# Kernel tuning notes

Measured on AMD Instinct MI355X. Metric: run time of the kernel, lower is better.

The kernel has to match this reference:

```python
import jax, jax.numpy as jnp
import numpy as np

N = 100000      # nodes
E = 1600000     # edges (avg degree 16)
D_IN, D_H, D_OUT = 128, 128, 64
EPS = 1e-5      # BatchNorm eps


def setup_inputs() -> dict:
    key = jax.random.key(0)
    ks = jax.random.split(key, 16)
    def w(k, i, o):
        return jax.random.normal(k, (i, o), jnp.float32) / np.float32(np.sqrt(i))
    inp = {
        "x": jax.random.normal(ks[0], (N, D_IN), jnp.float32),
        "edge_index": jax.random.randint(ks[1], (2, E), 0, N, dtype=jnp.int32),
        # layer 0 (SAGEConv: lin_l on aggregated neighbors w/ bias, lin_r on root w/o bias)
        "Wl0": w(ks[2], D_IN, D_H), "bl0": jax.random.normal(ks[3], (D_H,), jnp.float32) * 0.01,
        "Wr0": w(ks[4], D_IN, D_H),
        "g0": jnp.ones((D_H,), jnp.float32), "b0": jnp.zeros((D_H,), jnp.float32),
        "m0": jax.random.normal(ks[5], (D_H,), jnp.float32) * 0.1, "v0": jnp.ones((D_H,), jnp.float32),
        # layer 1
        "Wl1": w(ks[6], D_H, D_H), "bl1": jax.random.normal(ks[7], (D_H,), jnp.float32) * 0.01,
        "Wr1": w(ks[8], D_H, D_H),
        "g1": jnp.ones((D_H,), jnp.float32), "b1": jnp.zeros((D_H,), jnp.float32),
        "m1": jax.random.normal(ks[9], (D_H,), jnp.float32) * 0.1, "v1": jnp.ones((D_H,), jnp.float32),
        # layer 2 (output)
        "Wl2": w(ks[10], D_H, D_OUT), "bl2": jax.random.normal(ks[11], (D_OUT,), jnp.float32) * 0.01,
        "Wr2": w(ks[12], D_H, D_OUT),
    }
    return inp


def _sage_conv(x, src, dst, Wl, bl, Wr):
    # mean aggregation of neighbor (source) features at destination nodes
    deg = jax.ops.segment_sum(jnp.ones((src.shape[0],), x.dtype), dst, num_segments=N)
    agg = jax.ops.segment_sum(x[src], dst, num_segments=N)  # [N, d] irregular scatter-add
    agg = agg / jnp.maximum(deg, 1.0)[:, None]
    return agg @ Wl + bl + x @ Wr


def _bn(h, g, b, m, v):
    # BatchNorm1d in eval mode (running stats)
    return g * (h - m) * jax.lax.rsqrt(v + EPS) + b


def reference(x, edge_index,
              Wl0, bl0, Wr0, g0, b0, m0, v0,
              Wl1, bl1, Wr1, g1, b1, m1, v1,
              Wl2, bl2, Wr2):
    src, dst = edge_index[0], edge_index[1]
    h = jax.nn.relu(_bn(_sage_conv(x, src, dst, Wl0, bl0, Wr0), g0, b0, m0, v0))
    h = jax.nn.relu(_bn(_sage_conv(h, src, dst, Wl1, bl1, Wr1), g1, b1, m1, v1))
    h = _sage_conv(h, src, dst, Wl2, bl2, Wr2)
    return jax.nn.log_softmax(h, axis=-1)
```

## Files before the change

### kernel.cpp

```cpp
#include <hip/hip_runtime.h>

constexpr float EPS = 1e-5f;

#define NPB_LOG 9
#define NPB 512

typedef __attribute__((ext_vector_type(8))) __bf16 bf16x8;
typedef __attribute__((ext_vector_type(4))) float f32x4;
typedef __attribute__((ext_vector_type(2))) float f32x2;

__device__ __forceinline__ float blo(unsigned u) { return __uint_as_float(u << 16); }
__device__ __forceinline__ float bhi(unsigned u) { return __uint_as_float(u & 0xffff0000u); }
__device__ __forceinline__ unsigned bf1(float f) {
    unsigned u = __float_as_uint(f);
    return (u + 0x7fffu + ((u >> 16) & 1u)) >> 16;
}
__device__ __forceinline__ unsigned pack2(float a, float b) { return bf1(a) | (bf1(b) << 16); }

__device__ __forceinline__ f32x2 fp8lo(unsigned w) {
    return __builtin_amdgcn_cvt_pk_f32_fp8(w, false);
}
__device__ __forceinline__ f32x2 fp8hi(unsigned w) {
    return __builtin_amdgcn_cvt_pk_f32_fp8(w, true);
}


__global__ void bucket_hist_kernel(const int* __restrict__ dst, int* __restrict__ bcnt,
                                   int E, int B) {
    __shared__ int h[256];
    int t = threadIdx.x;
    h[t] = 0;
    __syncthreads();
    int E4 = E >> 2;
    const uint4* d4 = reinterpret_cast<const uint4*>(dst);
    for (int i = blockIdx.x * blockDim.x + t; i < E4; i += gridDim.x * blockDim.x) {
        uint4 d = d4[i];
        atomicAdd(&h[d.x >> NPB_LOG], 1);
        atomicAdd(&h[d.y >> NPB_LOG], 1);
        atomicAdd(&h[d.z >> NPB_LOG], 1);
        atomicAdd(&h[d.w >> NPB_LOG], 1);
    }
    if (blockIdx.x == 0 && t < (E & 3))
        atomicAdd(&h[dst[E4 * 4 + t] >> NPB_LOG], 1);
    __syncthreads();
    if (t < B && h[t]) atomicAdd(&bcnt[t], h[t]);
}

__global__ void bucket_scan_kernel(const int* __restrict__ bcnt, int* __restrict__ bstart,
                                   int* __restrict__ cursorB, int B, int E) {
    __shared__ int tmp[256];
    int t = threadIdx.x;
    int v = (t < B) ? bcnt[t] : 0;
    tmp[t] = v;
    __syncthreads();
    for (int off = 1; off < 256; off <<= 1) {
        int x = tmp[t];
        if (t >= off) x += tmp[t - off];
        __syncthreads();
        tmp[t] = x;
        __syncthreads();
    }
    if (t < B) {
        int ex = tmp[t] - v;
        bstart[t] = ex;
        cursorB[t] = ex;
    }
    if (t == 0) bstart[B] = E;
}

__global__ __launch_bounds__(256) void partition_kernel(
    const int* __restrict__ src, const int* __restrict__ dst,
    int* __restrict__ cursorB, unsigned* __restrict__ ebuf, int E, int B) {
    __shared__ int hist[256];
    __shared__ int base[256];
    int t = threadIdx.x;
    hist[t] = 0;
// ... 117 lines not shown
}

__device__ __forceinline__ void swz_one(const float* __restrict__ Wl, const float* __restrict__ Wr,
                                        unsigned short* __restrict__ out, int CL, int CR, int id) {
    int C = CL + CR;
    int CT = C >> 4;
    int lane = id & 63;
    int ctkt = id >> 6;
    int ct = ctkt % CT;
    int kt = ctkt / CT;
    int col = ct * 16 + (lane & 15);
    int k0 = kt * 32 + (lane >> 4) * 8;
#pragma unroll
    for (int i = 0; i < 8; ++i) {
        int k = k0 + i;
        float w = (col < CL) ? Wl[(size_t)k * CL + col] : Wr[(size_t)k * CR + (col - CL)];
        out[(size_t)id * 8 + i] = (unsigned short)bf1(w);
    }
}

__global__ void prep_kernel(const float* __restrict__ Wl0, const float* __restrict__ Wr0,
                            const float* __restrict__ Wl1, const float* __restrict__ Wr1,
                            const float* __restrict__ Wl2, const float* __restrict__ Wr2,
                            const float* __restrict__ g0, const float* __restrict__ b0,
                            const float* __restrict__ m0, const float* __restrict__ v0,
                            const float* __restrict__ g1, const float* __restrict__ b1,
                            const float* __restrict__ m1, const float* __restrict__ v1,
                            unsigned short* __restrict__ Wsw0, unsigned short* __restrict__ Wsw1,
                            unsigned short* __restrict__ Wsw2,
                            float* __restrict__ bnA0, float* __restrict__ bnB0,
                            float* __restrict__ bnA1, float* __restrict__ bnB1) {
    int bid = blockIdx.x;
    int t = threadIdx.x;
    if (bid < 16) {
        swz_one(Wl0, Wr0, Wsw0, 128, 128, bid * 256 + t);
    } else if (bid < 32) {
        swz_one(Wl1, Wr1, Wsw1, 128, 128, (bid - 16) * 256 + t);
    } else if (bid < 40) {
        swz_one(Wl2, Wr2, Wsw2, 64, 64, (bid - 32) * 256 + t);
    } else {
        if (t < 128) {
            float A = g0[t] * rsqrtf(v0[t] + EPS);
            bnA0[t] = A;
            bnB0[t] = b0[t] - m0[t] * A;
        } else {
            int c = t - 128;
            float A = g1[c] * rsqrtf(v1[c] + EPS);
            bnA1[c] = A;
            bnB1[c] = b1[c] - m1[c] * A;
        }
    }
}

template <int CHALF, bool AF32>
__global__ __launch_bounds__(256, 4) void gemmT_kernel(
    const void* __restrict__ Av, const unsigned short* __restrict__ Wsw,
    const float* __restrict__ bl,
    unsigned char* __restrict__ tL, unsigned short* __restrict__ tR, int n) {
    constexpr int CT = CHALF / 16;
    __shared__ unsigned short As[64][136];

    int tid = threadIdx.x;
    int lane = tid & 63;
    int wave = tid >> 6;
    int wr = wave >> 1, wc = wave & 1;
    int blk0 = blockIdx.x * 64;
    int rlo = lane & 15, kq = lane >> 4;

    {
        int srow = tid >> 2;
        int schunk = tid & 3;
        int grow = blk0 + srow;
        uint4 w0 = make_uint4(0, 0, 0, 0), w1 = w0, w2 = w0, w3 = w0;
        if (grow < n) {
            if (AF32) {
                const float* Af = (const float*)Av;
                const float4* p = reinterpret_cast<const float4*>(Af + (size_t)grow * 128 + schunk * 32);
                float4 f0 = p[0], f1 = p[1], f2 = p[2], f3 = p[3];
                float4 f4 = p[4], f5 = p[5], f6 = p[6], f7 = p[7];
                w0 = make_uint4(pack2(f0.x, f0.y), pack2(f0.z, f0.w), pack2(f1.x, f1.y), pack2(f1.z, f1.w));
                w1 = make_uint4(pack2(f2.x, f2.y), pack2(f2.z, f2.w), pack2(f3.x, f3.y), pack2(f3.z, f3.w));
                w2 = make_uint4(pack2(f4.x, f4.y), pack2(f4.z, f4.w), pack2(f5.x, f5.y), pack2(f5.z, f5.w));
                w3 = make_uint4(pack2(f6.x, f6.y), pack2(f6.z, f6.w), pack2(f7.x, f7.y), pack2(f7.z, f7.w));
            } else {
                const unsigned short* A = (const unsigned short*)Av;
                const uint4* p = reinterpret_cast<const uint4*>(A + (size_t)grow * 128 + schunk * 32);
                w0 = p[0]; w1 = p[1]; w2 = p[2]; w3 = p[3];
            }
        }
        uint4* d = reinterpret_cast<uint4*>(&As[srow][schunk * 32]);
        d[0] = w0; d[1] = w1; d[2] = w2; d[3] = w3;
    }
    __syncthreads();

    f32x4 acc[2][CT];
#pragma unroll
    for (int nt = 0; nt < 2; ++nt)
#pragma unroll
        for (int c = 0; c < CT; ++c)
#pragma unroll
            for (int k = 0; k < 4; ++k) acc[nt][c][k] = 0.f;

    int lr0 = wr * 32 + rlo;
    int lr1 = wr * 32 + 16 + rlo;

    for (int kt = 0; kt < 4; ++kt) {
        int kb = kt * 32 + kq * 8;
        bf16x8 a0 = *reinterpret_cast<const bf16x8*>(&As[lr0][kb]);
        bf16x8 a1 = *reinterpret_cast<const bf16x8*>(&As[lr1][kb]);
#pragma unroll
        for (int c = 0; c < CT; ++c) {
            int ct_g = wc * CT + c;
            bf16x8 w = *reinterpret_cast<const bf16x8*>(Wsw + ((size_t)(kt * 2 * CT + ct_g) * 64 + lane) * 8);
            acc[0][c] = __builtin_amdgcn_mfma_f32_16x16x32_bf16(w, a0, acc[0][c], 0, 0, 0);
            acc[1][c] = __builtin_amdgcn_mfma_f32_16x16x32_bf16(w, a1, acc[1][c], 0, 0, 0);
        }
    }

#pragma unroll
    for (int nt = 0; nt < 2; ++nt) {
        int r = blk0 + wr * 32 + nt * 16 + rlo;
        if (r >= n) continue;
#pragma unroll
        for (int c = 0; c < CT; ++c) {
            int colbase = c * 16 + kq * 4;
            if (wc == 0) {
                unsigned w = __builtin_amdgcn_cvt_pk_fp8_f32(acc[nt][c][0], acc[nt][c][1], 0, false);
                w = __builtin_amdgcn_cvt_pk_fp8_f32(acc[nt][c][2], acc[nt][c][3], w, true);
                *reinterpret_cast<unsigned*>(tL + (size_t)r * CHALF + colbase) = w;
            } else {
                float4 bv = *reinterpret_cast<const float4*>(bl + colbase);
                uint2 o;
                o.x = pack2(acc[nt][c][0] + bv.x, acc[nt][c][1] + bv.y);
                o.y = pack2(acc[nt][c][2] + bv.z, acc[nt][c][3] + bv.w);
                *reinterpret_cast<uint2*>(tR + (size_t)r * CHALF + colbase) = o;
            }
        }
    }
}

__global__ void aggbn_kernel(const unsigned char* __restrict__ tL,
                             const unsigned short* __restrict__ tR,
                             const float* __restrict__ bnA, const float* __restrict__ bnB,
                             const int* __restrict__ rowptr, const int* __restrict__ csr,
                             const float* __restrict__ degInv,
                             unsigned short* __restrict__ h, int n) {
    int idx = blockIdx.x * blockDim.x + threadIdx.x;
    int v = idx >> 4;
    int t = idx & 15;
    if (v >= n) return;
    int beg = rowptr[v], end = rowptr[v + 1];
    const uint2* T2 = reinterpret_cast<const uint2*>(tL);
    float s0 = 0.f, s1 = 0.f, s2 = 0.f, s3 = 0.f, s4 = 0.f, s5 = 0.f, s6 = 0.f, s7 = 0.f;
    int e = beg;
    for (; e + 8 <= end; e += 8) {
        uint2 w0 = T2[(size_t)csr[e + 0] * 16 + t];
        uint2 w1 = T2[(size_t)csr[e + 1] * 16 + t];
        uint2 w2 = T2[(size_t)csr[e + 2] * 16 + t];
        uint2 w3 = T2[(size_t)csr[e + 3] * 16 + t];
        uint2 w4 = T2[(size_t)csr[e + 4] * 16 + t];
        uint2 w5 = T2[(size_t)csr[e + 5] * 16 + t];
        uint2 w6 = T2[(size_t)csr[e + 6] * 16 + t];
        uint2 w7 = T2[(size_t)csr[e + 7] * 16 + t];
        f32x2 p;
        p = fp8lo(w0.x); s0 += p[0]; s1 += p[1];
        p = fp8hi(w0.x); s2 += p[0]; s3 += p[1];
        p = fp8lo(w0.y); s4 += p[0]; s5 += p[1];
        p = fp8hi(w0.y); s6 += p[0]; s7 += p[1];
        p = fp8lo(w1.x); s0 += p[0]; s1 += p[1];
        p = fp8hi(w1.x); s2 += p[0]; s3 += p[1];
        p = fp8lo(w1.y); s4 += p[0]; s5 += p[1];
        p = fp8hi(w1.y); s6 += p[0]; s7 += p[1];
        p = fp8lo(w2.x); s0 += p[0]; s1 += p[1];
        p = fp8hi(w2.x); s2 += p[0]; s3 += p[1];
        p = fp8lo(w2.y); s4 += p[0]; s5 += p[1];
        p = fp8hi(w2.y); s6 += p[0]; s7 += p[1];
        p = fp8lo(w3.x); s0 += p[0]; s1 += p[1];
        p = fp8hi(w3.x); s2 += p[0]; s3 += p[1];
        p = fp8lo(w3.y); s4 += p[0]; s5 += p[1];
        p = fp8hi(w3.y); s6 += p[0]; s7 += p[1];
        p = fp8lo(w4.x); s0 += p[0]; s1 += p[1];
        p = fp8hi(w4.x); s2 += p[0]; s3 += p[1];
        p = fp8lo(w4.y); s4 += p[0]; s5 += p[1];
        p = fp8hi(w4.y); s6 += p[0]; s7 += p[1];
        p = fp8lo(w5.x); s0 += p[0]; s1 += p[1];
        p = fp8hi(w5.x); s2 += p[0]; s3 += p[1];
        p = fp8lo(w5.y); s4 += p[0]; s5 += p[1];
        p = fp8hi(w5.y); s6 += p[0]; s7 += p[1];
        p = fp8lo(w6.x); s0 += p[0]; s1 += p[1];
        p = fp8hi(w6.x); s2 += p[0]; s3 += p[1];
        p = fp8lo(w6.y); s4 += p[0]; s5 += p[1];
        p = fp8hi(w6.y); s6 += p[0]; s7 += p[1];
        p = fp8lo(w7.x); s0 += p[0]; s1 += p[1];
        p = fp8hi(w7.x); s2 += p[0]; s3 += p[1];
        p = fp8lo(w7.y); s4 += p[0]; s5 += p[1];
        p = fp8hi(w7.y); s6 += p[0]; s7 += p[1];
    }
    for (; e < end; ++e) {
        uint2 w = T2[(size_t)csr[e] * 16 + t];
        f32x2 p;
        p = fp8lo(w.x); s0 += p[0]; s1 += p[1];
        p = fp8hi(w.x); s2 += p[0]; s3 += p[1];
        p = fp8lo(w.y); s4 += p[0]; s5 += p[1];
        p = fp8hi(w.y); s6 += p[0]; s7 += p[1];
    }
    float di = degInv[v];
    uint4 rw = reinterpret_cast<const uint4*>(tR)[(size_t)v * 16 + t];
    float4 A0 = reinterpret_cast<const float4*>(bnA + t * 8)[0];
    float4 A1 = reinterpret_cast<const float4*>(bnA + t * 8)[1];
    float4 B0 = reinterpret_cast<const float4*>(bnB + t * 8)[0];
    float4 B1 = reinterpret_cast<const float4*>(bnB + t * 8)[1];
    float h0 = fmaxf(A0.x * (s0 * di + blo(rw.x)) + B0.x, 0.f);
    float h1 = fmaxf(A0.y * (s1 * di + bhi(rw.x)) + B0.y, 0.f);
    float h2 = fmaxf(A0.z * (s2 * di + blo(rw.y)) + B0.z, 0.f);
    float h3 = fmaxf(A0.w * (s3 * di + bhi(rw.y)) + B0.w, 0.f);
    float h4 = fmaxf(A1.x * (s4 * di + blo(rw.z)) + B1.x, 0.f);
    float h5 = fmaxf(A1.y * (s5 * di + bhi(rw.z)) + B1.y, 0.f);
    float h6 = fmaxf(A1.z * (s6 * di + blo(rw.w)) + B1.z, 0.f);
    float h7 = fmaxf(A1.w * (s7 * di + bhi(rw.w)) + B1.w, 0.f);
    uint4 o;
    o.x = pack2(h0, h1);
    o.y = pack2(h2, h3);
    o.z = pack2(h4, h5);
    o.w = pack2(h6, h7);
    reinterpret_cast<uint4*>(h)[(size_t)v * 16 + t] = o;
}

__global__ void agg64_lsm_kernel(const unsigned char* __restrict__ tL2,
                                 const unsigned short* __restrict__ tR2,
                                 const int* __restrict__ rowptr, const int* __restrict__ csr,
                                 const float* __restrict__ degInv,
                                 float* __restrict__ out, int n) {
    int idx = blockIdx.x * blockDim.x + threadIdx.x;
    int v = idx >> 3;
    int t = idx & 7;
    if (v >= n) return;
    int beg = rowptr[v], end = rowptr[v + 1];
    const uint2* T2 = reinterpret_cast<const uint2*>(tL2);
    float s0 = 0.f, s1 = 0.f, s2 = 0.f, s3 = 0.f, s4 = 0.f, s5 = 0.f, s6 = 0.f, s7 = 0.f;
    int e = beg;
    for (; e + 8 <= end; e += 8) {
        uint2 w0 = T2[(size_t)csr[e + 0] * 8 + t];
        uint2 w1 = T2[(size_t)csr[e + 1] * 8 + t];
        uint2 w2 = T2[(size_t)csr[e + 2] * 8 + t];
        uint2 w3 = T2[(size_t)csr[e + 3] * 8 + t];
        uint2 w4 = T2[(size_t)csr[e + 4] * 8 + t];
        uint2 w5 = T2[(size_t)csr[e + 5] * 8 + t];
        uint2 w6 = T2[(size_t)csr[e + 6] * 8 + t];
        uint2 w7 = T2[(size_t)csr[e + 7] * 8 + t];
        f32x2 p;
        p = fp8lo(w0.x); s0 += p[0]; s1 += p[1];
        p = fp8hi(w0.x); s2 += p[0]; s3 += p[1];
        p = fp8lo(w0.y); s4 += p[0]; s5 += p[1];
        p = fp8hi(w0.y); s6 += p[0]; s7 += p[1];
        p = fp8lo(w1.x); s0 += p[0]; s1 += p[1];
        p = fp8hi(w1.x); s2 += p[0]; s3 += p[1];
        p = fp8lo(w1.y); s4 += p[0]; s5 += p[1];
        p = fp8hi(w1.y); s6 += p[0]; s7 += p[1];
        p = fp8lo(w2.x); s0 += p[0]; s1 += p[1];
        p = fp8hi(w2.x); s2 += p[0]; s3 += p[1];
        p = fp8lo(w2.y); s4 += p[0]; s5 += p[1];
        p = fp8hi(w2.y); s6 += p[0]; s7 += p[1];
        p = fp8lo(w3.x); s0 += p[0]; s1 += p[1];
        p = fp8hi(w3.x); s2 += p[0]; s3 += p[1];
        p = fp8lo(w3.y); s4 += p[0]; s5 += p[1];
        p = fp8hi(w3.y); s6 += p[0]; s7 += p[1];
        p = fp8lo(w4.x); s0 += p[0]; s1 += p[1];
        p = fp8hi(w4.x); s2 += p[0]; s3 += p[1];
        p = fp8lo(w4.y); s4 += p[0]; s5 += p[1];
        p = fp8hi(w4.y); s6 += p[0]; s7 += p[1];
        p = fp8lo(w5.x); s0 += p[0]; s1 += p[1];
        p = fp8hi(w5.x); s2 += p[0]; s3 += p[1];
        p = fp8lo(w5.y); s4 += p[0]; s5 += p[1];
        p = fp8hi(w5.y); s6 += p[0]; s7 += p[1];
        p = fp8lo(w6.x); s0 += p[0]; s1 += p[1];
        p = fp8hi(w6.x); s2 += p[0]; s3 += p[1];
        p = fp8lo(w6.y); s4 += p[0]; s5 += p[1];
        p = fp8hi(w6.y); s6 += p[0]; s7 += p[1];
// ... 34 lines not shown
    float4 oA, oB;
    oA.x = y0 - lse; oA.y = y1 - lse; oA.z = y2 - lse; oA.w = y3 - lse;
    oB.x = y4 - lse; oB.y = y5 - lse; oB.z = y6 - lse; oB.w = y7 - lse;
    float4* O4 = reinterpret_cast<float4*>(out + (size_t)v * 64 + t * 8);
    O4[0] = oA;
    O4[1] = oB;
}


extern "C" void kernel_launch(void* const* d_in, const int* in_sizes, int n_in,
                              void* d_out, int out_size, void* d_ws, size_t ws_size,
                              hipStream_t stream) {
    const float* x   = (const float*)d_in[0];
    const int*   ei  = (const int*)d_in[1];
    const float* Wl0 = (const float*)d_in[2];
    const float* bl0 = (const float*)d_in[3];
    const float* Wr0 = (const float*)d_in[4];
    const float* g0  = (const float*)d_in[5];
    const float* b0  = (const float*)d_in[6];
    const float* m0  = (const float*)d_in[7];
    const float* v0  = (const float*)d_in[8];
    const float* Wl1 = (const float*)d_in[9];
    const float* bl1 = (const float*)d_in[10];
    const float* Wr1 = (const float*)d_in[11];
    const float* g1  = (const float*)d_in[12];
    const float* b1  = (const float*)d_in[13];
    const float* m1  = (const float*)d_in[14];
    const float* v1  = (const float*)d_in[15];
    const float* Wl2 = (const float*)d_in[16];
    const float* bl2 = (const float*)d_in[17];
    const float* Wr2 = (const float*)d_in[18];
    float* out = (float*)d_out;

    const int N = in_sizes[0] / 128;
    const int E = in_sizes[1] / 2;
    const int B = (N + NPB - 1) >> NPB_LOG;
    const int* src = ei;
    const int* dst = ei + E;

    char* ws = (char*)d_ws;
    size_t off = 0;
    auto alloc = [&](size_t bytes) -> void* {
        void* p = ws + off;
        off += (bytes + 255) & ~(size_t)255;
        return p;
    };
    int*   bcnt    = (int*)alloc(256 * 4);
    int*   bstart  = (int*)alloc(257 * 4);
    int*   cursorB = (int*)alloc(256 * 4);
    int*   rowptr  = (int*)alloc((size_t)(N + 1) * 4);
    float* degInv  = (float*)alloc((size_t)N * 4);
    int*   csr     = (int*)alloc((size_t)E * 4);
    unsigned* ebuf = (unsigned*)alloc((size_t)E * 4);
    unsigned short* hA  = (unsigned short*)alloc((size_t)N * 128 * 2);
    unsigned short* hB  = (unsigned short*)alloc((size_t)N * 128 * 2);
    unsigned char*  tL  = (unsigned char*)alloc((size_t)N * 128);
    unsigned short* tR  = (unsigned short*)alloc((size_t)N * 128 * 2);
    unsigned short* Wsw0 = (unsigned short*)alloc(4 * 16 * 64 * 8 * 2);
    unsigned short* Wsw1 = (unsigned short*)alloc(4 * 16 * 64 * 8 * 2);
    unsigned short* Wsw2 = (unsigned short*)alloc(4 * 8 * 64 * 8 * 2);
    float* bnA0 = (float*)alloc(128 * 4);
    float* bnB0 = (float*)alloc(128 * 4);
    float* bnA1 = (float*)alloc(128 * 4);
    float* bnB1 = (float*)alloc(128 * 4);
    unsigned char*  tL2 = tL;
    unsigned short* tR2 = tR;

    hipMemsetAsync(bcnt, 0, 256 * 4, stream);

    bucket_hist_kernel<<<512, 256, 0, stream>>>(dst, bcnt, E, B);
    bucket_scan_kernel<<<1, 256, 0, stream>>>(bcnt, bstart, cursorB, B, E);
    partition_kernel<<<(E + 4095) / 4096, 256, 0, stream>>>(src, dst, cursorB, ebuf, E, B);
    build_csr_kernel<<<B, 256, 0, stream>>>(ebuf, bstart, rowptr, degInv, csr, N, B);
    prep_kernel<<<41, 256, 0, stream>>>(Wl0, Wr0, Wl1, Wr1, Wl2, Wr2,
                                        g0, b0, m0, v0, g1, b1, m1, v1,
                                        Wsw0, Wsw1, Wsw2, bnA0, bnB0, bnA1, bnB1);

    int gemmGrid = (N + 63) / 64;
    int aggGrid = (int)(((size_t)N * 16 + 255) / 256);
    int lsmGrid = (int)(((size_t)N * 8 + 255) / 256);

    gemmT_kernel<128, true><<<gemmGrid, 256, 0, stream>>>(x, Wsw0, bl0, tL, tR, N);
    aggbn_kernel<<<aggGrid, 256, 0, stream>>>(tL, tR, bnA0, bnB0, rowptr, csr, degInv, hA, N);
    gemmT_kernel<128, false><<<gemmGrid, 256, 0, stream>>>(hA, Wsw1, bl1, tL, tR, N);
    aggbn_kernel<<<aggGrid, 256, 0, stream>>>(tL, tR, bnA1, bnB1, rowptr, csr, degInv, hB, N);
    gemmT_kernel<64, false><<<gemmGrid, 256, 0, stream>>>(hB, Wsw2, bl2, tL2, tR2, N);
    agg64_lsm_kernel<<<lsmGrid, 256, 0, stream>>>(tL2, tR2, rowptr, csr, degInv, out, N);
}
```

Baseline: 247.0 us.

## Fuse neighbor aggregation and BatchNorm into the following layer's GEMM kernel

```diff
diff --git a/kernel.cpp b/kernel.cpp
--- a/kernel.cpp
+++ b/kernel.cpp
@@ -22,6 +22,19 @@
 }
 __device__ __forceinline__ f32x2 fp8hi(unsigned w) {
     return __builtin_amdgcn_cvt_pk_f32_fp8(w, true);
+}
+
+template <int B>
+__device__ __forceinline__ void acc16(float (&s)[32], uint4 w) {
+    f32x2 p;
+    p = fp8lo(w.x); s[B + 0] += p[0];  s[B + 1] += p[1];
+    p = fp8hi(w.x); s[B + 2] += p[0];  s[B + 3] += p[1];
+    p = fp8lo(w.y); s[B + 4] += p[0];  s[B + 5] += p[1];
+    p = fp8hi(w.y); s[B + 6] += p[0];  s[B + 7] += p[1];
+    p = fp8lo(w.z); s[B + 8] += p[0];  s[B + 9] += p[1];
+    p = fp8hi(w.z); s[B + 10] += p[0]; s[B + 11] += p[1];
+    p = fp8lo(w.w); s[B + 12] += p[0]; s[B + 13] += p[1];
+    p = fp8hi(w.w); s[B + 14] += p[0]; s[B + 15] += p[1];
 }
 
 
@@ -245,12 +258,11 @@
     }
 }
 
-template <int CHALF, bool AF32>
-__global__ __launch_bounds__(256, 4) void gemmT_kernel(
-    const void* __restrict__ Av, const unsigned short* __restrict__ Wsw,
+__global__ __launch_bounds__(256, 4) void gemm0_kernel(
+    const float* __restrict__ Af, const unsigned short* __restrict__ Wsw,
     const float* __restrict__ bl,
     unsigned char* __restrict__ tL, unsigned short* __restrict__ tR, int n) {
-    constexpr int CT = CHALF / 16;
+    constexpr int CT = 8;
     __shared__ unsigned short As[64][136];
 
     int tid = threadIdx.x;
@@ -266,20 +278,13 @@
         int grow = blk0 + srow;
         uint4 w0 = make_uint4(0, 0, 0, 0), w1 = w0, w2 = w0, w3 = w0;
         if (grow < n) {
-            if (AF32) {
-                const float* Af = (const float*)Av;
-                const float4* p = reinterpret_cast<const float4*>(Af + (size_t)grow * 128 + schunk * 32);
-                float4 f0 = p[0], f1 = p[1], f2 = p[2], f3 = p[3];
-                float4 f4 = p[4], f5 = p[5], f6 = p[6], f7 = p[7];
-                w0 = make_uint4(pack2(f0.x, f0.y), pack2(f0.z, f0.w), pack2(f1.x, f1.y), pack2(f1.z, f1.w));
-                w1 = make_uint4(pack2(f2.x, f2.y), pack2(f2.z, f2.w), pack2(f3.x, f3.y), pack2(f3.z, f3.w));
-                w2 = make_uint4(pack2(f4.x, f4.y), pack2(f4.z, f4.w), pack2(f5.x, f5.y), pack2(f5.z, f5.w));
-                w3 = make_uint4(pack2(f6.x, f6.y), pack2(f6.z, f6.w), pack2(f7.x, f7.y), pack2(f7.z, f7.w));
-            } else {
-                const unsigned short* A = (const unsigned short*)Av;
-                const uint4* p = reinterpret_cast<const uint4*>(A + (size_t)grow * 128 + schunk * 32);
-                w0 = p[0]; w1 = p[1]; w2 = p[2]; w3 = p[3];
-            }
+            const float4* p = reinterpret_cast<const float4*>(Af + (size_t)grow * 128 + schunk * 32);
+            float4 f0 = p[0], f1 = p[1], f2 = p[2], f3 = p[3];
+            float4 f4 = p[4], f5 = p[5], f6 = p[6], f7 = p[7];
+            w0 = make_uint4(pack2(f0.x, f0.y), pack2(f0.z, f0.w), pack2(f1.x, f1.y), pack2(f1.z, f1.w));
+            w1 = make_uint4(pack2(f2.x, f2.y), pack2(f2.z, f2.w), pack2(f3.x, f3.y), pack2(f3.z, f3.w));
+            w2 = make_uint4(pack2(f4.x, f4.y), pack2(f4.z, f4.w), pack2(f5.x, f5.y), pack2(f5.z, f5.w));
+            w3 = make_uint4(pack2(f6.x, f6.y), pack2(f6.z, f6.w), pack2(f7.x, f7.y), pack2(f7.z, f7.w));
         }
         uint4* d = reinterpret_cast<uint4*>(&As[srow][schunk * 32]);
         d[0] = w0; d[1] = w1; d[2] = w2; d[3] = w3;
@@ -320,103 +325,144 @@
             if (wc == 0) {
                 unsigned w = __builtin_amdgcn_cvt_pk_fp8_f32(acc[nt][c][0], acc[nt][c][1], 0, false);
                 w = __builtin_amdgcn_cvt_pk_fp8_f32(acc[nt][c][2], acc[nt][c][3], w, true);
-                *reinterpret_cast<unsigned*>(tL + (size_t)r * CHALF + colbase) = w;
+                *reinterpret_cast<unsigned*>(tL + (size_t)r * 128 + colbase) = w;
             } else {
                 float4 bv = *reinterpret_cast<const float4*>(bl + colbase);
                 uint2 o;
                 o.x = pack2(acc[nt][c][0] + bv.x, acc[nt][c][1] + bv.y);
                 o.y = pack2(acc[nt][c][2] + bv.z, acc[nt][c][3] + bv.w);
-                *reinterpret_cast<uint2*>(tR + (size_t)r * CHALF + colbase) = o;
+                *reinterpret_cast<uint2*>(tR + (size_t)r * 128 + colbase) = o;
             }
         }
     }
 }
 
-__global__ void aggbn_kernel(const unsigned char* __restrict__ tL,
-                             const unsigned short* __restrict__ tR,
-                             const float* __restrict__ bnA, const float* __restrict__ bnB,
-                             const int* __restrict__ rowptr, const int* __restrict__ csr,
-                             const float* __restrict__ degInv,
-                             unsigned short* __restrict__ h, int n) {
-    int idx = blockIdx.x * blockDim.x + threadIdx.x;
-    int v = idx >> 4;
-    int t = idx & 15;
-    if (v >= n) return;
-    int beg = rowptr[v], end = rowptr[v + 1];
-    const uint2* T2 = reinterpret_cast<const uint2*>(tL);
-    float s0 = 0.f, s1 = 0.f, s2 = 0.f, s3 = 0.f, s4 = 0.f, s5 = 0.f, s6 = 0.f, s7 = 0.f;
-    int e = beg;
-    for (; e + 8 <= end; e += 8) {
-        uint2 w0 = T2[(size_t)csr[e + 0] * 16 + t];
-        uint2 w1 = T2[(size_t)csr[e + 1] * 16 + t];
-        uint2 w2 = T2[(size_t)csr[e + 2] * 16 + t];
-        uint2 w3 = T2[(size_t)csr[e + 3] * 16 + t];
-        uint2 w4 = T2[(size_t)csr[e + 4] * 16 + t];
-        uint2 w5 = T2[(size_t)csr[e + 5] * 16 + t];
-        uint2 w6 = T2[(size_t)csr[e + 6] * 16 + t];
-        uint2 w7 = T2[(size_t)csr[e + 7] * 16 + t];
-        f32x2 p;
-        p = fp8lo(w0.x); s0 += p[0]; s1 += p[1];
-        p = fp8hi(w0.x); s2 += p[0]; s3 += p[1];
-        p = fp8lo(w0.y); s4 += p[0]; s5 += p[1];
-        p = fp8hi(w0.y); s6 += p[0]; s7 += p[1];
-        p = fp8lo(w1.x); s0 += p[0]; s1 += p[1];
-        p = fp8hi(w1.x); s2 += p[0]; s3 += p[1];
-        p = fp8lo(w1.y); s4 += p[0]; s5 += p[1];
-        p = fp8hi(w1.y); s6 += p[0]; s7 += p[1];
-        p = fp8lo(w2.x); s0 += p[0]; s1 += p[1];
-        p = fp8hi(w2.x); s2 += p[0]; s3 += p[1];
-        p = fp8lo(w2.y); s4 += p[0]; s5 += p[1];
-        p = fp8hi(w2.y); s6 += p[0]; s7 += p[1];
-        p = fp8lo(w3.x); s0 += p[0]; s1 += p[1];
-        p = fp8hi(w3.x); s2 += p[0]; s3 += p[1];
-        p = fp8lo(w3.y); s4 += p[0]; s5 += p[1];
-        p = fp8hi(w3.y); s6 += p[0]; s7 += p[1];
-        p = fp8lo(w4.x); s0 += p[0]; s1 += p[1];
-        p = fp8hi(w4.x); s2 += p[0]; s3 += p[1];
-        p = fp8lo(w4.y); s4 += p[0]; s5 += p[1];
-        p = fp8hi(w4.y); s6 += p[0]; s7 += p[1];
-        p = fp8lo(w5.x); s0 += p[0]; s1 += p[1];
-        p = fp8hi(w5.x); s2 += p[0]; s3 += p[1];
-        p = fp8lo(w5.y); s4 += p[0]; s5 += p[1];
-        p = fp8hi(w5.y); s6 += p[0]; s7 += p[1];
-        p = fp8lo(w6.x); s0 += p[0]; s1 += p[1];
-        p = fp8hi(w6.x); s2 += p[0]; s3 += p[1];
-        p = fp8lo(w6.y); s4 += p[0]; s5 += p[1];
-        p = fp8hi(w6.y); s6 += p[0]; s7 += p[1];
-        p = fp8lo(w7.x); s0 += p[0]; s1 += p[1];
-        p = fp8hi(w7.x); s2 += p[0]; s3 += p[1];
-        p = fp8lo(w7.y); s4 += p[0]; s5 += p[1];
-        p = fp8hi(w7.y); s6 += p[0]; s7 += p[1];
-    }
-    for (; e < end; ++e) {
-        uint2 w = T2[(size_t)csr[e] * 16 + t];
-        f32x2 p;
-        p = fp8lo(w.x); s0 += p[0]; s1 += p[1];
-        p = fp8hi(w.x); s2 += p[0]; s3 += p[1];
-        p = fp8lo(w.y); s4 += p[0]; s5 += p[1];
-        p = fp8hi(w.y); s6 += p[0]; s7 += p[1];
-    }
-    float di = degInv[v];
-    uint4 rw = reinterpret_cast<const uint4*>(tR)[(size_t)v * 16 + t];
-    float4 A0 = reinterpret_cast<const float4*>(bnA + t * 8)[0];
-    float4 A1 = reinterpret_cast<const float4*>(bnA + t * 8)[1];
-    float4 B0 = reinterpret_cast<const float4*>(bnB + t * 8)[0];
-    float4 B1 = reinterpret_cast<const float4*>(bnB + t * 8)[1];
-    float h0 = fmaxf(A0.x * (s0 * di + blo(rw.x)) + B0.x, 0.f);
-    float h1 = fmaxf(A0.y * (s1 * di + bhi(rw.x)) + B0.y, 0.f);
-    float h2 = fmaxf(A0.z * (s2 * di + blo(rw.y)) + B0.z, 0.f);
-    float h3 = fmaxf(A0.w * (s3 * di + bhi(rw.y)) + B0.w, 0.f);
-    float h4 = fmaxf(A1.x * (s4 * di + blo(rw.z)) + B1.x, 0.f);
-    float h5 = fmaxf(A1.y * (s5 * di + bhi(rw.z)) + B1.y, 0.f);
-    float h6 = fmaxf(A1.z * (s6 * di + blo(rw.w)) + B1.z, 0.f);
-    float h7 = fmaxf(A1.w * (s7 * di + bhi(rw.w)) + B1.w, 0.f);
-    uint4 o;
-    o.x = pack2(h0, h1);
-    o.y = pack2(h2, h3);
-    o.z = pack2(h4, h5);
-    o.w = pack2(h6, h7);
-    reinterpret_cast<uint4*>(h)[(size_t)v * 16 + t] = o;
+template <int CHALF>
+__global__ __launch_bounds__(256, 4) void fusedAG_kernel(
+    const unsigned char* __restrict__ tLin, const unsigned short* __restrict__ tRin,
+    const float* __restrict__ bnA, const float* __restrict__ bnB,
+    const int* __restrict__ rowptr, const int* __restrict__ csr,
+    const float* __restrict__ degInv,
+    const unsigned short* __restrict__ Wsw, const float* __restrict__ bl,
+    unsigned char* __restrict__ tLout, unsigned short* __restrict__ tRout, int n) {
+    constexpr int CT = CHALF / 16;
+    __shared__ unsigned short As[64][136];
+
+    int tid = threadIdx.x;
+    int blk0 = blockIdx.x * 64;
+
+    {
+        int lrow = tid >> 2;
+        int t = tid & 3;
+        int v = blk0 + lrow;
+        uint4* dst = reinterpret_cast<uint4*>(&As[lrow][t * 32]);
+        if (v < n) {
+            float s[32];
+#pragma unroll
+            for (int j = 0; j < 32; ++j) s[j] = 0.f;
+            int beg = rowptr[v], end = rowptr[v + 1];
+            const uint4* T4 = reinterpret_cast<const uint4*>(tLin);
+            int e = beg;
+            for (; e + 4 <= end; e += 4) {
+                const uint4* r0 = T4 + (size_t)csr[e + 0] * 8 + t * 2;
+                const uint4* r1 = T4 + (size_t)csr[e + 1] * 8 + t * 2;
+                const uint4* r2 = T4 + (size_t)csr[e + 2] * 8 + t * 2;
+                const uint4* r3 = T4 + (size_t)csr[e + 3] * 8 + t * 2;
+                uint4 a0 = r0[0], a1 = r0[1];
+                uint4 b0 = r1[0], b1 = r1[1];
+                uint4 c0 = r2[0], c1 = r2[1];
+                uint4 d0 = r3[0], d1 = r3[1];
+                acc16<0>(s, a0); acc16<16>(s, a1);
+                acc16<0>(s, b0); acc16<16>(s, b1);
+                acc16<0>(s, c0); acc16<16>(s, c1);
+                acc16<0>(s, d0); acc16<16>(s, d1);
+            }
+            for (; e < end; ++e) {
+                const uint4* r0 = T4 + (size_t)csr[e] * 8 + t * 2;
+                uint4 a0 = r0[0], a1 = r0[1];
+                acc16<0>(s, a0); acc16<16>(s, a1);
+            }
+            float di = degInv[v];
+            const uint4* R4 = reinterpret_cast<const uint4*>(tRin + (size_t)v * 128 + t * 32);
+            uint4 rr[4] = { R4[0], R4[1], R4[2], R4[3] };
+            const float4* A4 = reinterpret_cast<const float4*>(bnA + t * 32);
+            const float4* B4 = reinterpret_cast<const float4*>(bnB + t * 32);
+#pragma unroll
+            for (int j = 0; j < 4; ++j) {
+                uint4 rj = rr[j];
+                float4 Aa = A4[2 * j], Ab = A4[2 * j + 1];
+                float4 Ba = B4[2 * j], Bb = B4[2 * j + 1];
+                float h0 = fmaxf(Aa.x * (s[8 * j + 0] * di + blo(rj.x)) + Ba.x, 0.f);
+                float h1 = fmaxf(Aa.y * (s[8 * j + 1] * di + bhi(rj.x)) + Ba.y, 0.f);
+                float h2 = fmaxf(Aa.z * (s[8 * j + 2] * di + blo(rj.y)) + Ba.z, 0.f);
+                float h3 = fmaxf(Aa.w * (s[8 * j + 3] * di + bhi(rj.y)) + Ba.w, 0.f);
+                float h4 = fmaxf(Ab.x * (s[8 * j + 4] * di + blo(rj.z)) + Bb.x, 0.f);
+                float h5 = fmaxf(Ab.y * (s[8 * j + 5] * di + bhi(rj.z)) + Bb.y, 0.f);
+                float h6 = fmaxf(Ab.z * (s[8 * j + 6] * di + blo(rj.w)) + Bb.z, 0.f);
+                float h7 = fmaxf(Ab.w * (s[8 * j + 7] * di + bhi(rj.w)) + Bb.w, 0.f);
+                uint4 o;
+                o.x = pack2(h0, h1);
+                o.y = pack2(h2, h3);
+                o.z = pack2(h4, h5);
+                o.w = pack2(h6, h7);
+                dst[j] = o;
+            }
+        } else {
+            uint4 z = make_uint4(0, 0, 0, 0);
+            dst[0] = z; dst[1] = z; dst[2] = z; dst[3] = z;
+        }
+    }
+    __syncthreads();
+
+    int lane = tid & 63;
+    int wave = tid >> 6;
+    int wr = wave >> 1, wc = wave & 1;
+    int rlo = lane & 15, kq = lane >> 4;
+
+    f32x4 acc[2][CT];
+#pragma unroll
+    for (int nt = 0; nt < 2; ++nt)
+#pragma unroll
+        for (int c = 0; c < CT; ++c)
+#pragma unroll
+            for (int k = 0; k < 4; ++k) acc[nt][c][k] = 0.f;
+
+    int lr0 = wr * 32 + rlo;
+    int lr1 = wr * 32 + 16 + rlo;
+
+    for (int kt = 0; kt < 4; ++kt) {
+        int kb = kt * 32 + kq * 8;
+        bf16x8 a0 = *reinterpret_cast<const bf16x8*>(&As[lr0][kb]);
+        bf16x8 a1 = *reinterpret_cast<const bf16x8*>(&As[lr1][kb]);
+#pragma unroll
+        for (int c = 0; c < CT; ++c) {
+            int ct_g = wc * CT + c;
+            bf16x8 w = *reinterpret_cast<const bf16x8*>(Wsw + ((size_t)(kt * 2 * CT + ct_g) * 64 + lane) * 8);
+            acc[0][c] = __builtin_amdgcn_mfma_f32_16x16x32_bf16(w, a0, acc[0][c], 0, 0, 0);
+            acc[1][c] = __builtin_amdgcn_mfma_f32_16x16x32_bf16(w, a1, acc[1][c], 0, 0, 0);
+        }
+    }
+
+#pragma unroll
+    for (int nt = 0; nt < 2; ++nt) {
+        int r = blk0 + wr * 32 + nt * 16 + rlo;
+        if (r >= n) continue;
+#pragma unroll
+        for (int c = 0; c < CT; ++c) {
+            int colbase = c * 16 + kq * 4;
+            if (wc == 0) {
+                unsigned w = __builtin_amdgcn_cvt_pk_fp8_f32(acc[nt][c][0], acc[nt][c][1], 0, false);
+                w = __builtin_amdgcn_cvt_pk_fp8_f32(acc[nt][c][2], acc[nt][c][3], w, true);
+                *reinterpret_cast<unsigned*>(tLout + (size_t)r * CHALF + colbase) = w;
+            } else {
+                float4 bv = *reinterpret_cast<const float4*>(bl + colbase);
+                uint2 o;
+                o.x = pack2(acc[nt][c][0] + bv.x, acc[nt][c][1] + bv.y);
+                o.y = pack2(acc[nt][c][2] + bv.z, acc[nt][c][3] + bv.w);
+                *reinterpret_cast<uint2*>(tRout + (size_t)r * CHALF + colbase) = o;
+            }
+        }
+    }
 }
 
 __global__ void agg64_lsm_kernel(const unsigned char* __restrict__ tL2,
@@ -557,10 +603,10 @@
     float* degInv  = (float*)alloc((size_t)N * 4);
     int*   csr     = (int*)alloc((size_t)E * 4);
     unsigned* ebuf = (unsigned*)alloc((size_t)E * 4);
-    unsigned short* hA  = (unsigned short*)alloc((size_t)N * 128 * 2);
-    unsigned short* hB  = (unsigned short*)alloc((size_t)N * 128 * 2);
-    unsigned char*  tL  = (unsigned char*)alloc((size_t)N * 128);
-    unsigned short* tR  = (unsigned short*)alloc((size_t)N * 128 * 2);
+    unsigned char*  tLa = (unsigned char*)alloc((size_t)N * 128);
+    unsigned short* tRa = (unsigned short*)alloc((size_t)N * 128 * 2);
+    unsigned char*  tLb = (unsigned char*)alloc((size_t)N * 128);
+    unsigned short* tRb = (unsigned short*)alloc((size_t)N * 128 * 2);
     unsigned short* Wsw0 = (unsigned short*)alloc(4 * 16 * 64 * 8 * 2);
     unsigned short* Wsw1 = (unsigned short*)alloc(4 * 16 * 64 * 8 * 2);
     unsigned short* Wsw2 = (unsigned short*)alloc(4 * 8 * 64 * 8 * 2);
@@ -568,8 +614,8 @@
     float* bnB0 = (float*)alloc(128 * 4);
     float* bnA1 = (float*)alloc(128 * 4);
     float* bnB1 = (float*)alloc(128 * 4);
-    unsigned char*  tL2 = tL;
-    unsigned short* tR2 = tR;
+    unsigned char*  tL2 = tLa;
+    unsigned short* tR2 = tRa;
 
     hipMemsetAsync(bcnt, 0, 256 * 4, stream);
 
@@ -582,13 +628,12 @@
                                         Wsw0, Wsw1, Wsw2, bnA0, bnB0, bnA1, bnB1);
 
     int gemmGrid = (N + 63) / 64;
-    int aggGrid = (int)(((size_t)N * 16 + 255) / 256);
     int lsmGrid = (int)(((size_t)N * 8 + 255) / 256);
 
-    gemmT_kernel<128, true><<<gemmGrid, 256, 0, stream>>>(x, Wsw0, bl0, tL, tR, N);
-    aggbn_kernel<<<aggGrid, 256, 0, stream>>>(tL, tR, bnA0, bnB0, rowptr, csr, degInv, hA, N);
-    gemmT_kernel<128, false><<<gemmGrid, 256, 0, stream>>>(hA, Wsw1, bl1, tL, tR, N);
-    aggbn_kernel<<<aggGrid, 256, 0, stream>>>(tL, tR, bnA1, bnB1, rowptr, csr, degInv, hB, N);
-    gemmT_kernel<64, false><<<gemmGrid, 256, 0, stream>>>(hB, Wsw2, bl2, tL2, tR2, N);
+    gemm0_kernel<<<gemmGrid, 256, 0, stream>>>(x, Wsw0, bl0, tLa, tRa, N);
+    fusedAG_kernel<128><<<gemmGrid, 256, 0, stream>>>(
+        tLa, tRa, bnA0, bnB0, rowptr, csr, degInv, Wsw1, bl1, tLb, tRb, N);
+    fusedAG_kernel<64><<<gemmGrid, 256, 0, stream>>>(
+        tLb, tRb, bnA1, bnB1, rowptr, csr, degInv, Wsw2, bl2, tL2, tR2, N);
     agg64_lsm_kernel<<<lsmGrid, 256, 0, stream>>>(tL2, tR2, rowptr, csr, degInv, out, N);
 }
```

Measured after the change: 413.9 us. +67.6%, slower.

## Fuse neighbor aggregation + BatchNorm with following layer GEMM via LDS tile

Applied to the files above, without the earlier changes.

```diff
diff --git a/kernel.cpp b/kernel.cpp
--- a/kernel.cpp
+++ b/kernel.cpp
@@ -245,12 +245,11 @@
     }
 }
 
-template <int CHALF, bool AF32>
-__global__ __launch_bounds__(256, 4) void gemmT_kernel(
-    const void* __restrict__ Av, const unsigned short* __restrict__ Wsw,
+__global__ __launch_bounds__(256, 4) void gemm0_kernel(
+    const float* __restrict__ Af, const unsigned short* __restrict__ Wsw,
     const float* __restrict__ bl,
     unsigned char* __restrict__ tL, unsigned short* __restrict__ tR, int n) {
-    constexpr int CT = CHALF / 16;
+    constexpr int CT = 8;
     __shared__ unsigned short As[64][136];
 
     int tid = threadIdx.x;
@@ -266,20 +265,13 @@
         int grow = blk0 + srow;
         uint4 w0 = make_uint4(0, 0, 0, 0), w1 = w0, w2 = w0, w3 = w0;
         if (grow < n) {
-            if (AF32) {
-                const float* Af = (const float*)Av;
-                const float4* p = reinterpret_cast<const float4*>(Af + (size_t)grow * 128 + schunk * 32);
-                float4 f0 = p[0], f1 = p[1], f2 = p[2], f3 = p[3];
-                float4 f4 = p[4], f5 = p[5], f6 = p[6], f7 = p[7];
-                w0 = make_uint4(pack2(f0.x, f0.y), pack2(f0.z, f0.w), pack2(f1.x, f1.y), pack2(f1.z, f1.w));
-                w1 = make_uint4(pack2(f2.x, f2.y), pack2(f2.z, f2.w), pack2(f3.x, f3.y), pack2(f3.z, f3.w));
-                w2 = make_uint4(pack2(f4.x, f4.y), pack2(f4.z, f4.w), pack2(f5.x, f5.y), pack2(f5.z, f5.w));
-                w3 = make_uint4(pack2(f6.x, f6.y), pack2(f6.z, f6.w), pack2(f7.x, f7.y), pack2(f7.z, f7.w));
-            } else {
-                const unsigned short* A = (const unsigned short*)Av;
-                const uint4* p = reinterpret_cast<const uint4*>(A + (size_t)grow * 128 + schunk * 32);
-                w0 = p[0]; w1 = p[1]; w2 = p[2]; w3 = p[3];
-            }
+            const float4* p = reinterpret_cast<const float4*>(Af + (size_t)grow * 128 + schunk * 32);
+            float4 f0 = p[0], f1 = p[1], f2 = p[2], f3 = p[3];
+            float4 f4 = p[4], f5 = p[5], f6 = p[6], f7 = p[7];
+            w0 = make_uint4(pack2(f0.x, f0.y), pack2(f0.z, f0.w), pack2(f1.x, f1.y), pack2(f1.z, f1.w));
+            w1 = make_uint4(pack2(f2.x, f2.y), pack2(f2.z, f2.w), pack2(f3.x, f3.y), pack2(f3.z, f3.w));
+            w2 = make_uint4(pack2(f4.x, f4.y), pack2(f4.z, f4.w), pack2(f5.x, f5.y), pack2(f5.z, f5.w));
+            w3 = make_uint4(pack2(f6.x, f6.y), pack2(f6.z, f6.w), pack2(f7.x, f7.y), pack2(f7.z, f7.w));
         }
         uint4* d = reinterpret_cast<uint4*>(&As[srow][schunk * 32]);
         d[0] = w0; d[1] = w1; d[2] = w2; d[3] = w3;
@@ -320,103 +312,169 @@
             if (wc == 0) {
                 unsigned w = __builtin_amdgcn_cvt_pk_fp8_f32(acc[nt][c][0], acc[nt][c][1], 0, false);
                 w = __builtin_amdgcn_cvt_pk_fp8_f32(acc[nt][c][2], acc[nt][c][3], w, true);
-                *reinterpret_cast<unsigned*>(tL + (size_t)r * CHALF + colbase) = w;
+                *reinterpret_cast<unsigned*>(tL + (size_t)r * 128 + colbase) = w;
             } else {
                 float4 bv = *reinterpret_cast<const float4*>(bl + colbase);
                 uint2 o;
                 o.x = pack2(acc[nt][c][0] + bv.x, acc[nt][c][1] + bv.y);
                 o.y = pack2(acc[nt][c][2] + bv.z, acc[nt][c][3] + bv.w);
-                *reinterpret_cast<uint2*>(tR + (size_t)r * CHALF + colbase) = o;
+                *reinterpret_cast<uint2*>(tR + (size_t)r * 128 + colbase) = o;
             }
         }
     }
 }
 
-__global__ void aggbn_kernel(const unsigned char* __restrict__ tL,
-                             const unsigned short* __restrict__ tR,
-                             const float* __restrict__ bnA, const float* __restrict__ bnB,
-                             const int* __restrict__ rowptr, const int* __restrict__ csr,
-                             const float* __restrict__ degInv,
-                             unsigned short* __restrict__ h, int n) {
-    int idx = blockIdx.x * blockDim.x + threadIdx.x;
-    int v = idx >> 4;
-    int t = idx & 15;
-    if (v >= n) return;
-    int beg = rowptr[v], end = rowptr[v + 1];
-    const uint2* T2 = reinterpret_cast<const uint2*>(tL);
-    float s0 = 0.f, s1 = 0.f, s2 = 0.f, s3 = 0.f, s4 = 0.f, s5 = 0.f, s6 = 0.f, s7 = 0.f;
-    int e = beg;
-    for (; e + 8 <= end; e += 8) {
-        uint2 w0 = T2[(size_t)csr[e + 0] * 16 + t];
-        uint2 w1 = T2[(size_t)csr[e + 1] * 16 + t];
-        uint2 w2 = T2[(size_t)csr[e + 2] * 16 + t];
-        uint2 w3 = T2[(size_t)csr[e + 3] * 16 + t];
-        uint2 w4 = T2[(size_t)csr[e + 4] * 16 + t];
-        uint2 w5 = T2[(size_t)csr[e + 5] * 16 + t];
-        uint2 w6 = T2[(size_t)csr[e + 6] * 16 + t];
-        uint2 w7 = T2[(size_t)csr[e + 7] * 16 + t];
-        f32x2 p;
-        p = fp8lo(w0.x); s0 += p[0]; s1 += p[1];
-        p = fp8hi(w0.x); s2 += p[0]; s3 += p[1];
-        p = fp8lo(w0.y); s4 += p[0]; s5 += p[1];
-        p = fp8hi(w0.y); s6 += p[0]; s7 += p[1];
-        p = fp8lo(w1.x); s0 += p[0]; s1 += p[1];
-        p = fp8hi(w1.x); s2 += p[0]; s3 += p[1];
-        p = fp8lo(w1.y); s4 += p[0]; s5 += p[1];
-        p = fp8hi(w1.y); s6 += p[0]; s7 += p[1];
-        p = fp8lo(w2.x); s0 += p[0]; s1 += p[1];
-        p = fp8hi(w2.x); s2 += p[0]; s3 += p[1];
-        p = fp8lo(w2.y); s4 += p[0]; s5 += p[1];
-        p = fp8hi(w2.y); s6 += p[0]; s7 += p[1];
-        p = fp8lo(w3.x); s0 += p[0]; s1 += p[1];
-        p = fp8hi(w3.x); s2 += p[0]; s3 += p[1];
-        p = fp8lo(w3.y); s4 += p[0]; s5 += p[1];
-        p = fp8hi(w3.y); s6 += p[0]; s7 += p[1];
-        p = fp8lo(w4.x); s0 += p[0]; s1 += p[1];
-        p = fp8hi(w4.x); s2 += p[0]; s3 += p[1];
-        p = fp8lo(w4.y); s4 += p[0]; s5 += p[1];
-        p = fp8hi(w4.y); s6 += p[0]; s7 += p[1];
-        p = fp8lo(w5.x); s0 += p[0]; s1 += p[1];
-        p = fp8hi(w5.x); s2 += p[0]; s3 += p[1];
-        p = fp8lo(w5.y); s4 += p[0]; s5 += p[1];
-        p = fp8hi(w5.y); s6 += p[0]; s7 += p[1];
-        p = fp8lo(w6.x); s0 += p[0]; s1 += p[1];
-        p = fp8hi(w6.x); s2 += p[0]; s3 += p[1];
-        p = fp8lo(w6.y); s4 += p[0]; s5 += p[1];
-        p = fp8hi(w6.y); s6 += p[0]; s7 += p[1];
-        p = fp8lo(w7.x); s0 += p[0]; s1 += p[1];
-        p = fp8hi(w7.x); s2 += p[0]; s3 += p[1];
-        p = fp8lo(w7.y); s4 += p[0]; s5 += p[1];
-        p = fp8hi(w7.y); s6 += p[0]; s7 += p[1];
-    }
-    for (; e < end; ++e) {
-        uint2 w = T2[(size_t)csr[e] * 16 + t];
-        f32x2 p;
-        p = fp8lo(w.x); s0 += p[0]; s1 += p[1];
-        p = fp8hi(w.x); s2 += p[0]; s3 += p[1];
-        p = fp8lo(w.y); s4 += p[0]; s5 += p[1];
-        p = fp8hi(w.y); s6 += p[0]; s7 += p[1];
-    }
-    float di = degInv[v];
-    uint4 rw = reinterpret_cast<const uint4*>(tR)[(size_t)v * 16 + t];
-    float4 A0 = reinterpret_cast<const float4*>(bnA + t * 8)[0];
-    float4 A1 = reinterpret_cast<const float4*>(bnA + t * 8)[1];
-    float4 B0 = reinterpret_cast<const float4*>(bnB + t * 8)[0];
-    float4 B1 = reinterpret_cast<const float4*>(bnB + t * 8)[1];
-    float h0 = fmaxf(A0.x * (s0 * di + blo(rw.x)) + B0.x, 0.f);
-    float h1 = fmaxf(A0.y * (s1 * di + bhi(rw.x)) + B0.y, 0.f);
-    float h2 = fmaxf(A0.z * (s2 * di + blo(rw.y)) + B0.z, 0.f);
-    float h3 = fmaxf(A0.w * (s3 * di + bhi(rw.y)) + B0.w, 0.f);
-    float h4 = fmaxf(A1.x * (s4 * di + blo(rw.z)) + B1.x, 0.f);
-    float h5 = fmaxf(A1.y * (s5 * di + bhi(rw.z)) + B1.y, 0.f);
-    float h6 = fmaxf(A1.z * (s6 * di + blo(rw.w)) + B1.z, 0.f);
-    float h7 = fmaxf(A1.w * (s7 * di + bhi(rw.w)) + B1.w, 0.f);
-    uint4 o;
-    o.x = pack2(h0, h1);
-    o.y = pack2(h2, h3);
-    o.z = pack2(h4, h5);
-    o.w = pack2(h6, h7);
-    reinterpret_cast<uint4*>(h)[(size_t)v * 16 + t] = o;
+template <int CHALF>
+__global__ __launch_bounds__(256) void fusedAG_kernel(
+    const unsigned char* __restrict__ tLin, const unsigned short* __restrict__ tRin,
+    const float* __restrict__ bnA, const float* __restrict__ bnB,
+    const int* __restrict__ rowptr, const int* __restrict__ csr,
+    const float* __restrict__ degInv,
+    const unsigned short* __restrict__ Wsw, const float* __restrict__ bl,
+    unsigned char* __restrict__ tLout, unsigned short* __restrict__ tRout, int n) {
+    constexpr int CT = CHALF / 16;
+    __shared__ unsigned short As[64][136];
+
+    int tid = threadIdx.x;
+    int blk0 = blockIdx.x * 64;
+    int t = tid & 15;
+    const uint2* T2 = reinterpret_cast<const uint2*>(tLin);
+
+#pragma unroll
+    for (int pass = 0; pass < 4; ++pass) {
+        int lrow = pass * 16 + (tid >> 4);
+        int v = blk0 + lrow;
+        uint4* dst = reinterpret_cast<uint4*>(&As[lrow][t * 8]);
+        if (v < n) {
+            float s0 = 0.f, s1 = 0.f, s2 = 0.f, s3 = 0.f, s4 = 0.f, s5 = 0.f, s6 = 0.f, s7 = 0.f;
+            int beg = rowptr[v], end = rowptr[v + 1];
+            int e = beg;
+            for (; e + 8 <= end; e += 8) {
+                uint2 w0 = T2[(size_t)csr[e + 0] * 16 + t];
+                uint2 w1 = T2[(size_t)csr[e + 1] * 16 + t];
+                uint2 w2 = T2[(size_t)csr[e + 2] * 16 + t];
+                uint2 w3 = T2[(size_t)csr[e + 3] * 16 + t];
+                uint2 w4 = T2[(size_t)csr[e + 4] * 16 + t];
+                uint2 w5 = T2[(size_t)csr[e + 5] * 16 + t];
+                uint2 w6 = T2[(size_t)csr[e + 6] * 16 + t];
+                uint2 w7 = T2[(size_t)csr[e + 7] * 16 + t];
+                f32x2 p;
+                p = fp8lo(w0.x); s0 += p[0]; s1 += p[1];
+                p = fp8hi(w0.x); s2 += p[0]; s3 += p[1];
+                p = fp8lo(w0.y); s4 += p[0]; s5 += p[1];
+                p = fp8hi(w0.y); s6 += p[0]; s7 += p[1];
+                p = fp8lo(w1.x); s0 += p[0]; s1 += p[1];
+                p = fp8hi(w1.x); s2 += p[0]; s3 += p[1];
+                p = fp8lo(w1.y); s4 += p[0]; s5 += p[1];
+                p = fp8hi(w1.y); s6 += p[0]; s7 += p[1];
+                p = fp8lo(w2.x); s0 += p[0]; s1 += p[1];
+                p = fp8hi(w2.x); s2 += p[0]; s3 += p[1];
+                p = fp8lo(w2.y); s4 += p[0]; s5 += p[1];
+                p = fp8hi(w2.y); s6 += p[0]; s7 += p[1];
+                p = fp8lo(w3.x); s0 += p[0]; s1 += p[1];
+                p = fp8hi(w3.x); s2 += p[0]; s3 += p[1];
+                p = fp8lo(w3.y); s4 += p[0]; s5 += p[1];
+                p = fp8hi(w3.y); s6 += p[0]; s7 += p[1];
+                p = fp8lo(w4.x); s0 += p[0]; s1 += p[1];
+                p = fp8hi(w4.x); s2 += p[0]; s3 += p[1];
+                p = fp8lo(w4.y); s4 += p[0]; s5 += p[1];
+                p = fp8hi(w4.y); s6 += p[0]; s7 += p[1];
+                p = fp8lo(w5.x); s0 += p[0]; s1 += p[1];
+                p = fp8hi(w5.x); s2 += p[0]; s3 += p[1];
+                p = fp8lo(w5.y); s4 += p[0]; s5 += p[1];
+                p = fp8hi(w5.y); s6 += p[0]; s7 += p[1];
+                p = fp8lo(w6.x); s0 += p[0]; s1 += p[1];
+                p = fp8hi(w6.x); s2 += p[0]; s3 += p[1];
+                p = fp8lo(w6.y); s4 += p[0]; s5 += p[1];
+                p = fp8hi(w6.y); s6 += p[0]; s7 += p[1];
+                p = fp8lo(w7.x); s0 += p[0]; s1 += p[1];
+                p = fp8hi(w7.x); s2 += p[0]; s3 += p[1];
+                p = fp8lo(w7.y); s4 += p[0]; s5 += p[1];
+                p = fp8hi(w7.y); s6 += p[0]; s7 += p[1];
+            }
+            for (; e < end; ++e) {
+                uint2 w = T2[(size_t)csr[e] * 16 + t];
+                f32x2 p;
+                p = fp8lo(w.x); s0 += p[0]; s1 += p[1];
+                p = fp8hi(w.x); s2 += p[0]; s3 += p[1];
+                p = fp8lo(w.y); s4 += p[0]; s5 += p[1];
+                p = fp8hi(w.y); s6 += p[0]; s7 += p[1];
+            }
+            float di = degInv[v];
+            uint4 rw = reinterpret_cast<const uint4*>(tRin)[(size_t)v * 16 + t];
+            float4 A0 = reinterpret_cast<const float4*>(bnA + t * 8)[0];
+            float4 A1 = reinterpret_cast<const float4*>(bnA + t * 8)[1];
+            float4 B0 = reinterpret_cast<const float4*>(bnB + t * 8)[0];
+            float4 B1 = reinterpret_cast<const float4*>(bnB + t * 8)[1];
+            float h0 = fmaxf(A0.x * (s0 * di + blo(rw.x)) + B0.x, 0.f);
+            float h1 = fmaxf(A0.y * (s1 * di + bhi(rw.x)) + B0.y, 0.f);
+            float h2 = fmaxf(A0.z * (s2 * di + blo(rw.y)) + B0.z, 0.f);
+            float h3 = fmaxf(A0.w * (s3 * di + bhi(rw.y)) + B0.w, 0.f);
+            float h4 = fmaxf(A1.x * (s4 * di + blo(rw.z)) + B1.x, 0.f);
+            float h5 = fmaxf(A1.y * (s5 * di + bhi(rw.z)) + B1.y, 0.f);
+            float h6 = fmaxf(A1.z * (s6 * di + blo(rw.w)) + B1.z, 0.f);
+            float h7 = fmaxf(A1.w * (s7 * di + bhi(rw.w)) + B1.w, 0.f);
+            uint4 o;
+            o.x = pack2(h0, h1);
+            o.y = pack2(h2, h3);
+            o.z = pack2(h4, h5);
+            o.w = pack2(h6, h7);
+            *dst = o;
+        } else {
+            *dst = make_uint4(0, 0, 0, 0);
+        }
+    }
+    __syncthreads();
+
+    int lane = tid & 63;
+    int wave = tid >> 6;
+    int wr = wave >> 1, wc = wave & 1;
+    int rlo = lane & 15, kq = lane >> 4;
+
+    f32x4 acc[2][CT];
+#pragma unroll
+    for (int nt = 0; nt < 2; ++nt)
+#pragma unroll
+        for (int c = 0; c < CT; ++c)
+#pragma unroll
+            for (int k = 0; k < 4; ++k) acc[nt][c][k] = 0.f;
+
+    int lr0 = wr * 32 + rlo;
+    int lr1 = wr * 32 + 16 + rlo;
+
+    for (int kt = 0; kt < 4; ++kt) {
+        int kb = kt * 32 + kq * 8;
+        bf16x8 a0 = *reinterpret_cast<const bf16x8*>(&As[lr0][kb]);
+        bf16x8 a1 = *reinterpret_cast<const bf16x8*>(&As[lr1][kb]);
+#pragma unroll
+        for (int c = 0; c < CT; ++c) {
+            int ct_g = wc * CT + c;
+            bf16x8 w = *reinterpret_cast<const bf16x8*>(Wsw + ((size_t)(kt * 2 * CT + ct_g) * 64 + lane) * 8);
+            acc[0][c] = __builtin_amdgcn_mfma_f32_16x16x32_bf16(w, a0, acc[0][c], 0, 0, 0);
+            acc[1][c] = __builtin_amdgcn_mfma_f32_16x16x32_bf16(w, a1, acc[1][c], 0, 0, 0);
+        }
+    }
+
+#pragma unroll
+    for (int nt = 0; nt < 2; ++nt) {
+        int r = blk0 + wr * 32 + nt * 16 + rlo;
+        if (r >= n) continue;
+#pragma unroll
+        for (int c = 0; c < CT; ++c) {
+            int colbase = c * 16 + kq * 4;
+            if (wc == 0) {
+                unsigned w = __builtin_amdgcn_cvt_pk_fp8_f32(acc[nt][c][0], acc[nt][c][1], 0, false);
+                w = __builtin_amdgcn_cvt_pk_fp8_f32(acc[nt][c][2], acc[nt][c][3], w, true);
+                *reinterpret_cast<unsigned*>(tLout + (size_t)r * CHALF + colbase) = w;
+            } else {
+                float4 bv = *reinterpret_cast<const float4*>(bl + colbase);
+                uint2 o;
+                o.x = pack2(acc[nt][c][0] + bv.x, acc[nt][c][1] + bv.y);
+                o.y = pack2(acc[nt][c][2] + bv.z, acc[nt][c][3] + bv.w);
+                *reinterpret_cast<uint2*>(tRout + (size_t)r * CHALF + colbase) = o;
+            }
+        }
+    }
 }
 
 __global__ void agg64_lsm_kernel(const unsigned char* __restrict__ tL2,
@@ -557,10 +615,10 @@
     float* degInv  = (float*)alloc((size_t)N * 4);
     int*   csr     = (int*)alloc((size_t)E * 4);
     unsigned* ebuf = (unsigned*)alloc((size_t)E * 4);
-    unsigned short* hA  = (unsigned short*)alloc((size_t)N * 128 * 2);
-    unsigned short* hB  = (unsigned short*)alloc((size_t)N * 128 * 2);
-    unsigned char*  tL  = (unsigned char*)alloc((size_t)N * 128);
-    unsigned short* tR  = (unsigned short*)alloc((size_t)N * 128 * 2);
+    unsigned char*  tLa = (unsigned char*)alloc((size_t)N * 128);
+    unsigned short* tRa = (unsigned short*)alloc((size_t)N * 128 * 2);
+    unsigned char*  tLb = (unsigned char*)alloc((size_t)N * 128);
+    unsigned short* tRb = (unsigned short*)alloc((size_t)N * 128 * 2);
     unsigned short* Wsw0 = (unsigned short*)alloc(4 * 16 * 64 * 8 * 2);
     unsigned short* Wsw1 = (unsigned short*)alloc(4 * 16 * 64 * 8 * 2);
     unsigned short* Wsw2 = (unsigned short*)alloc(4 * 8 * 64 * 8 * 2);
@@ -568,8 +626,8 @@
     float* bnB0 = (float*)alloc(128 * 4);
     float* bnA1 = (float*)alloc(128 * 4);
     float* bnB1 = (float*)alloc(128 * 4);
-    unsigned char*  tL2 = tL;
-    unsigned short* tR2 = tR;
+    unsigned char*  tL2 = tLa;
+    unsigned short* tR2 = tRa;
 
     hipMemsetAsync(bcnt, 0, 256 * 4, stream);
 
@@ -582,13 +640,12 @@
                                         Wsw0, Wsw1, Wsw2, bnA0, bnB0, bnA1, bnB1);
 
     int gemmGrid = (N + 63) / 64;
-    int aggGrid = (int)(((size_t)N * 16 + 255) / 256);
     int lsmGrid = (int)(((size_t)N * 8 + 255) / 256);
 
-    gemmT_kernel<128, true><<<gemmGrid, 256, 0, stream>>>(x, Wsw0, bl0, tL, tR, N);
-    aggbn_kernel<<<aggGrid, 256, 0, stream>>>(tL, tR, bnA0, bnB0, rowptr, csr, degInv, hA, N);
-    gemmT_kernel<128, false><<<gemmGrid, 256, 0, stream>>>(hA, Wsw1, bl1, tL, tR, N);
-    aggbn_kernel<<<aggGrid, 256, 0, stream>>>(tL, tR, bnA1, bnB1, rowptr, csr, degInv, hB, N);
-    gemmT_kernel<64, false><<<gemmGrid, 256, 0, stream>>>(hB, Wsw2, bl2, tL2, tR2, N);
+    gemm0_kernel<<<gemmGrid, 256, 0, stream>>>(x, Wsw0, bl0, tLa, tRa, N);
+    fusedAG_kernel<128><<<gemmGrid, 256, 0, stream>>>(
+        tLa, tRa, bnA0, bnB0, rowptr, csr, degInv, Wsw1, bl1, tLb, tRb, N);
+    fusedAG_kernel<64><<<gemmGrid, 256, 0, stream>>>(
+        tLb, tRb, bnA1, bnB1, rowptr, csr, degInv, Wsw2, bl2, tL2, tR2, N);
     agg64_lsm_kernel<<<lsmGrid, 256, 0, stream>>>(tL2, tR2, rowptr, csr, degInv, out, N);
 }
```

Result: slower. 342.0 us (+38.5%).
